# Performance work log

Hardware: AMD Instinct MI355X
Metric: run time of the kernel (lower is better)

## Reference

```python
import jax, jax.numpy as jnp
import numpy as np

N, MAX_NB, H, L, V, B, M = 16384, 15, 512, 128, 1024, 256, 65536


def setup_inputs() -> dict:
    key = jax.random.key(0)
    ks = jax.random.split(key, 32)
    s = 0.02  # param init scale
    inp = {
        'x_ids': jax.random.randint(ks[0], (N,), 0, V, dtype=jnp.int32),
        'contexts': jax.random.randint(ks[1], (N,), 0, B, dtype=jnp.int32),
        'nei_idx': jax.random.randint(ks[2], (N, MAX_NB), 0, M, dtype=jnp.int32),
        'nei_mask': jax.random.randint(ks[3], (N, MAX_NB), 0, 2, dtype=jnp.int32),
        'o_idx': jax.random.randint(ks[4], (N, MAX_NB), 0, M, dtype=jnp.int32),
        'o_mask': jax.random.randint(ks[5], (N, MAX_NB), 0, 2, dtype=jnp.int32),
        'H_msg': jax.random.normal(ks[6], (M, H), jnp.float32),
        'x_tree_vecs': jax.random.normal(ks[7], (B, L), jnp.float32),
        'embedding': jax.random.normal(ks[8], (V, H), jnp.float32) * s,
        'Wz_w': jax.random.normal(ks[9], (H, 2 * H), jnp.float32) * s,
        'Wz_b': jnp.zeros((H,), jnp.float32),
        'Wr_w': jax.random.normal(ks[10], (H, H), jnp.float32) * s,
        'Wr_b': jnp.zeros((H,), jnp.float32),
        'Ur_w': jax.random.normal(ks[11], (H, H), jnp.float32) * s,
        'Wh_w': jax.random.normal(ks[12], (H, 2 * H), jnp.float32) * s,
        'Wh_b': jnp.zeros((H,), jnp.float32),
        'W_w': jax.random.normal(ks[13], (H, H + L), jnp.float32) * s,
        'W_b': jnp.zeros((H,), jnp.float32),
        'Wo_w': jax.random.normal(ks[14], (V, H), jnp.float32) * s,
        'Wo_b': jnp.zeros((V,), jnp.float32),
        'Ui_w': jax.random.normal(ks[15], (H, 2 * H), jnp.float32) * s,
        'Ui_b': jnp.zeros((H,), jnp.float32),
        'U_w': jax.random.normal(ks[16], (H, H + L), jnp.float32) * s,
        'U_b': jnp.zeros((H,), jnp.float32),
        'Uo_w': jax.random.normal(ks[17], (1, H), jnp.float32) * s,
        'Uo_b': jnp.zeros((1,), jnp.float32),
    }
    return inp


def _gru(x, h_nei, Wz_w, Wz_b, Wr_w, Wr_b, Ur_w, Wh_w, Wh_b):
    # x: [N,H], h_nei: [N,MAX_NB,H]
    sum_h = h_nei.sum(axis=1)
    z = jax.nn.sigmoid(jnp.concatenate([x, sum_h], axis=1) @ Wz_w.T + Wz_b)
    r1 = (x @ Wr_w.T + Wr_b)[:, None, :]          # [N,1,H]
    r2 = jnp.einsum('nkh,gh->nkg', h_nei, Ur_w)   # U_r(h_nei), no bias
    r = jax.nn.sigmoid(r1 + r2)
    sum_gated = (r * h_nei).sum(axis=1)
    pre_h = jnp.tanh(jnp.concatenate([x, sum_gated], axis=1) @ Wh_w.T + Wh_b)
    return (1.0 - z) * sum_h + z * pre_h


def reference(x_ids, contexts, nei_idx, nei_mask, o_idx, o_mask, H_msg,
              x_tree_vecs, embedding, Wz_w, Wz_b, Wr_w, Wr_b, Ur_w,
              Wh_w, Wh_b, W_w, W_b, Wo_w, Wo_b, Ui_w, Ui_b, U_w, U_b,
              Uo_w, Uo_b):
    x = embedding[x_ids]                                   # [N,H]
    h_nei = H_msg[nei_idx] * nei_mask[..., None].astype(H_msg.dtype)  # [N,NB,H]
    o_nei = H_msg[o_idx] * o_mask[..., None].astype(H_msg.dtype)
    new_h = _gru(x, h_nei, Wz_w, Wz_b, Wr_w, Wr_b, Ur_w, Wh_w, Wh_b)
    cur_o = o_nei.sum(axis=1)                              # [N,H]
    ctx = x_tree_vecs[contexts]                            # [N,L]
    # word prediction: aggregate(new_h, contexts, x_tree_vecs, 'word')
    w_hid = jax.nn.relu(jnp.concatenate([new_h, ctx], axis=1) @ W_w.T + W_b)
    word_scores = w_hid @ Wo_w.T + Wo_b                    # [N,V]
    # stop prediction: U_i(cat(x, cur_o)) -> aggregate(..., 'stop')
    stop_h = jax.nn.relu(jnp.concatenate([x, cur_o], axis=1) @ Ui_w.T + Ui_b)
    s_hid = jax.nn.relu(jnp.concatenate([stop_h, ctx], axis=1) @ U_w.T + U_b)
    stop_scores = s_hid @ Uo_w.T + Uo_b                    # [N,1]
    return jnp.concatenate([word_scores, stop_scores], axis=1)  # [N,V+1]
```

## Files before the change

kernel.cpp:

```cpp
#include <hip/hip_runtime.h>
#include <hip/hip_bf16.h>

typedef unsigned short u16;
typedef unsigned int u32;
typedef __attribute__((ext_vector_type(8))) short s8v;
typedef __attribute__((ext_vector_type(4))) float f4v;

#define HDIM 512
#define NNODE 16384
#define NB 15

__device__ __forceinline__ u16 f2bu(float x) {
  union { float f; u32 i; } v; v.f = x;
  u32 r = v.i + 0x7FFFu + ((v.i >> 16) & 1u);
  return (u16)(r >> 16);
}
__device__ __forceinline__ float bu2f(u16 u) {
  union { u32 i; float f; } v; v.i = ((u32)u) << 16;
  return v.f;
}
__device__ __forceinline__ u32 pk(float a, float b) {
  return (u32)f2bu(a) | ((u32)f2bu(b) << 16);
}
__device__ __forceinline__ float sigm(float x) {
  return __builtin_amdgcn_rcpf(1.f + __expf(-x));
}
__device__ __forceinline__ void gl16(const void* g, void* l) {
  __builtin_amdgcn_global_load_lds(
      (const __attribute__((address_space(1))) u32*)g,
      (__attribute__((address_space(3))) u32*)l, 16, 0, 0);
}
template<int N> __device__ __forceinline__ void wait_vm() {
  if constexpr (N == 0) asm volatile("s_waitcnt vmcnt(0)" ::: "memory");
  else if constexpr (N == 2) asm volatile("s_waitcnt vmcnt(2)" ::: "memory");
  else asm volatile("s_waitcnt vmcnt(4)" ::: "memory");
}

__global__ __launch_bounds__(256) void k_cvt_all(
    const float* Wz_w, const float* Wr_w, const float* Wh_w, const float* Ui_w,
    const float* Ur_w, const float* W_w, const float* U_w, const float* Wo_w,
    const float* emb, const float* xtree,
    const float* Wz_b, const float* Wr_b, const float* Wh_b, const float* Ui_b,
    const float* W_b, const float* U_b,
    u16* wcat, u16* wz_h, u16* wh_h, u16* ui_h, u16* ur, u16* w_n, u16* u_n,
    u16* ccat, u16* wo, u16* emb_bf, u16* xt_bf, float* ebias, float* cbias) {
  int seg = blockIdx.y;
  const float* src = nullptr; u16* dst = nullptr;
  const float* fsrc = nullptr; float* fdst = nullptr;
  int R = 0, Cs = 0, c0 = 0, C = 0, fn = 0;
  switch (seg) {
    case 0:  src = Wz_w; dst = wcat;              R = 512;  Cs = 1024; c0 = 0;   C = 512; break;
    case 1:  src = Wr_w; dst = wcat + 512 * 512;  R = 512;  Cs = 512;  c0 = 0;   C = 512; break;
    case 2:  src = Wh_w; dst = wcat + 1024 * 512; R = 512;  Cs = 1024; c0 = 0;   C = 512; break;
    case 3:  src = Ui_w; dst = wcat + 1536 * 512; R = 512;  Cs = 1024; c0 = 0;   C = 512; break;
    case 4:  src = Wz_w; dst = wz_h;              R = 512;  Cs = 1024; c0 = 512; C = 512; break;
    case 5:  src = Wh_w; dst = wh_h;              R = 512;  Cs = 1024; c0 = 512; C = 512; break;
    case 6:  src = Ui_w; dst = ui_h;              R = 512;  Cs = 1024; c0 = 512; C = 512; break;
    case 7:  src = Ur_w; dst = ur;                R = 512;  Cs = 512;  c0 = 0;   C = 512; break;
    case 8:  src = W_w;  dst = w_n;               R = 512;  Cs = 640;  c0 = 0;   C = 512; break;
    case 9:  src = U_w;  dst = u_n;               R = 512;  Cs = 640;  c0 = 0;   C = 512; break;
    case 10: src = W_w;  dst = ccat;              R = 512;  Cs = 640;  c0 = 512; C = 128; break;
    case 11: src = U_w;  dst = ccat + 512 * 128;  R = 512;  Cs = 640;  c0 = 512; C = 128; break;
    case 12: src = Wo_w; dst = wo;                R = 1024; Cs = 512;  c0 = 0;   C = 512; break;
    case 13: src = emb;  dst = emb_bf;            R = 1024; Cs = 512;  c0 = 0;   C = 512; break;
    case 14: src = xtree; dst = xt_bf;            R = 256;  Cs = 128;  c0 = 0;   C = 128; break;
    case 15: fsrc = Wz_b; fdst = ebias;        fn = 512; break;
    case 16: fsrc = Wr_b; fdst = ebias + 512;  fn = 512; break;
    case 17: fsrc = Wh_b; fdst = ebias + 1024; fn = 512; break;
    case 18: fsrc = Ui_b; fdst = ebias + 1536; fn = 512; break;
    case 19: fsrc = W_b;  fdst = cbias;        fn = 512; break;
    case 20: fsrc = U_b;  fdst = cbias + 512;  fn = 512; break;
  }
  int i = blockIdx.x * 256 + threadIdx.x;
  if (fdst) { if (i < fn) fdst[i] = fsrc[i]; return; }
  int e0 = i * 8;
  if (e0 >= R * C) return;
  int r = e0 / C, c = e0 - r * C;
  const float* s = src + (size_t)r * Cs + c0 + c;
  float4 a = *reinterpret_cast<const float4*>(s);
  float4 b = *reinterpret_cast<const float4*>(s + 4);
  uint4 o = {pk(a.x, a.y), pk(a.z, a.w), pk(b.x, b.y), pk(b.z, b.w)};
  *reinterpret_cast<uint4*>(&dst[e0]) = o;
}

__global__ void k_cvtH(const float* __restrict__ src, u16* __restrict__ HR) {
  size_t i = ((size_t)blockIdx.x * 256 + threadIdx.x) * 8;
  size_t m = i >> 9, c = i & 511;
  float4 a = *reinterpret_cast<const float4*>(src + i);
  float4 b = *reinterpret_cast<const float4*>(src + i + 4);
  uint4 o = {pk(a.x, a.y), pk(a.z, a.w), pk(b.x, b.y), pk(b.z, b.w)};
  *reinterpret_cast<uint4*>(&HR[m * 1024 + c]) = o;
}

struct GP {
  const u16* A; const u16* B; int K; int lda;
  const float* gadd; int ldg; const int* gidx;
  const float* bias; const u16* shb;
  float* outf; u16* outh; int ldo;
};

template<int EP>
__device__ __forceinline__ void epi(int row, int col, float v, const GP& g) {
  if constexpr (EP == 0) {
    g.outf[(size_t)row * g.ldo + col] = v + (g.bias ? g.bias[col] : 0.f);
  } else if constexpr (EP == 3) {
    float pre = v + g.gadd[(size_t)g.gidx[row] * g.ldg + col];
    g.outh[(size_t)row * g.ldo + col] = f2bu(pre > 0.f ? pre : 0.f);
  } else {
    g.outh[(size_t)row * g.ldo + col] = f2bu(v);
  }
}

template<int EP, int KV>
__device__ void gemm_core(const GP& g, u16* AsB, u16* BsB) {
  const int tid = threadIdx.x, lane = tid & 63, w = tid >> 6;
  const int wm = (w >> 2) * 64, wn = (w & 3) * 32;
  const int nx = gridDim.x;
  int orig = blockIdx.y * nx + blockIdx.x;
  int q = (nx * gridDim.y) >> 3;
  int tile = (orig & 7) * q + (orig >> 3);
  const int n0 = (tile % nx) * 128, m0 = (tile / nx) * 128;

  const int sr = tid >> 2, sc = (tid & 3) ^ (sr & 3);
  const u16* gA = g.A + (size_t)(m0 + sr) * g.lda + sc * 8;
  const u16* gB = g.B + (size_t)(n0 + sr) * KV + sc * 8;
  const int ls = tid * 8;

  f4v acc[4][2];
  f4v z4 = {0.f, 0.f, 0.f, 0.f};
#pragma unroll
  for (int a = 0; a < 4; a++) { acc[a][0] = z4; acc[a][1] = z4; }

  constexpr int T = KV / 32;
  auto STAGE = [&](int t) {
    int buf = (t & 3) * 4096;
    gl16(gA + t * 32, AsB + buf + ls);
    gl16(gB + t * 32, BsB + buf + ls);
  };
  STAGE(0); STAGE(1); STAGE(2);

#pragma unroll
  for (int t = 0; t < T; t++) {
    if (t < T - 2) wait_vm<4>();
    else if (t == T - 2) wait_vm<2>();
    else wait_vm<0>();
    __builtin_amdgcn_s_barrier();
    asm volatile("" ::: "memory");
    if (t + 3 < T) STAGE(t + 3);
    const u16* as = AsB + (t & 3) * 4096;
    const u16* bs = BsB + (t & 3) * 4096;
    s8v af[4], bf[2];
    int cc = lane >> 4;
#pragma unroll
    for (int i = 0; i < 4; i++) {
      int R = wm + i * 16 + (lane & 15);
      af[i] = *reinterpret_cast<const s8v*>(&as[R * 32 + (cc ^ (R & 3)) * 8]);
    }
#pragma unroll
    for (int i = 0; i < 2; i++) {
      int C = wn + i * 16 + (lane & 15);
      bf[i] = *reinterpret_cast<const s8v*>(&bs[C * 32 + (cc ^ (C & 3)) * 8]);
    }
    __builtin_amdgcn_s_setprio(1);
#pragma unroll
    for (int mi = 0; mi < 4; mi++)
#pragma unroll
      for (int ni = 0; ni < 2; ni++)
        acc[mi][ni] = __builtin_amdgcn_mfma_f32_16x16x32_bf16(
            af[mi], bf[ni], acc[mi][ni], 0, 0, 0);
    __builtin_amdgcn_s_setprio(0);
  }
#pragma unroll
  for (int mi = 0; mi < 4; mi++)
#pragma unroll
    for (int ni = 0; ni < 2; ni++)
#pragma unroll
      for (int r = 0; r < 4; r++) {
        int row = m0 + wm + mi * 16 + (lane >> 4) * 4 + r;
        int col = n0 + wn + ni * 16 + (lane & 15);
        epi<EP>(row, col, acc[mi][ni][r], g);
      }
}

template<int EP, int KV>
__global__ __launch_bounds__(512, 4) void k_gemm(GP g) {
  __shared__ u16 As[4 * 4096], Bs[4 * 4096];
  gemm_core<EP, KV>(g, As, Bs);
}

template<int EPa, int EPb, int KV>
__global__ __launch_bounds__(512, 4) void k_pair(GP a, GP b) {
  __shared__ u16 As[4 * 4096], Bs[4 * 4096];
  if (blockIdx.z == 0) gemm_core<EPa, KV>(a, As, Bs);
  else gemm_core<EPb, KV>(b, As, Bs);
}

__global__ __launch_bounds__(512, 4) void k_znp(
    const u16* __restrict__ sumh, const u16* __restrict__ sg,
    const u16* __restrict__ Wz, const u16* __restrict__ Wh,
    const float* __restrict__ E_z, const float* __restrict__ E_h, int ldg,
    const int* __restrict__ gidx, u16* __restrict__ newh, GP gs) {
  __shared__ u16 S[32768];
  if (blockIdx.z == 1) { gemm_core<3, 512>(gs, S, S + 16384); return; }
  u16* As1 = S; u16* Bs1 = S + 8192;
  u16* As2 = S + 16384; u16* Bs2 = S + 24576;
  const int tid = threadIdx.x, lane = tid & 63, w = tid >> 6;
  const int wm = (w >> 2) * 64, wn = (w & 3) * 32;
  const int nx = gridDim.x;
  int orig = blockIdx.y * nx + blockIdx.x;
  int q = (nx * gridDim.y) >> 3;
  int tile = (orig & 7) * q + (orig >> 3);
  const int n0 = (tile % nx) * 128, m0 = (tile / nx) * 128;

  const u16 *gA1[2], *gA2[2], *gB1[2], *gB2[2]; int ls[2];
#pragma unroll
  for (int i = 0; i < 2; i++) {
    int slot = tid + i * 512;
    int r = slot >> 3, c = (slot & 7) ^ (r & 7);
    gA1[i] = sumh + (size_t)(m0 + r) * HDIM + c * 8;
    gA2[i] = sg + (size_t)(m0 + r) * HDIM + c * 8;
    gB1[i] = Wz + (size_t)(n0 + r) * HDIM + c * 8;
    gB2[i] = Wh + (size_t)(n0 + r) * HDIM + c * 8;
    ls[i] = slot * 8;
  }

  f4v az[4][2], ah[4][2];
  f4v z4 = {0.f, 0.f, 0.f, 0.f};
#pragma unroll
  for (int a = 0; a < 4; a++) {
    az[a][0] = z4; az[a][1] = z4; ah[a][0] = z4; ah[a][1] = z4;
  }

  for (int k0 = 0; k0 < HDIM; k0 += 64) {
    __syncthreads();
#pragma unroll
    for (int i = 0; i < 2; i++) gl16(gA1[i] + k0, As1 + ls[i]);
#pragma unroll
    for (int i = 0; i < 2; i++) gl16(gB1[i] + k0, Bs1 + ls[i]);
#pragma unroll
    for (int i = 0; i < 2; i++) gl16(gA2[i] + k0, As2 + ls[i]);
#pragma unroll
    for (int i = 0; i < 2; i++) gl16(gB2[i] + k0, Bs2 + ls[i]);
    __syncthreads();
#pragma unroll
    for (int ks = 0; ks < 2; ks++) {
      int cc = ks * 4 + (lane >> 4);
      {
        s8v af[4], bf[2];
#pragma unroll
        for (int i = 0; i < 4; i++) {
          int R = wm + i * 16 + (lane & 15);
          af[i] = *reinterpret_cast<const s8v*>(&As1[R * 64 + (cc ^ (R & 7)) * 8]);
        }
#pragma unroll
        for (int i = 0; i < 2; i++) {
          int C = wn + i * 16 + (lane & 15);
          bf[i] = *reinterpret_cast<const s8v*>(&Bs1[C * 64 + (cc ^ (C & 7)) * 8]);
        }
        __builtin_amdgcn_s_setprio(1);
#pragma unroll
        for (int mi = 0; mi < 4; mi++)
#pragma unroll
          for (int ni = 0; ni < 2; ni++)
            az[mi][ni] = __builtin_amdgcn_mfma_f32_16x16x32_bf16(
                af[mi], bf[ni], az[mi][ni], 0, 0, 0);
        __builtin_amdgcn_s_setprio(0);
      }
      {
        s8v af[4], bf[2];
#pragma unroll
        for (int i = 0; i < 4; i++) {
          int R = wm + i * 16 + (lane & 15);
          af[i] = *reinterpret_cast<const s8v*>(&As2[R * 64 + (cc ^ (R & 7)) * 8]);
        }
#pragma unroll
        for (int i = 0; i < 2; i++) {
          int C = wn + i * 16 + (lane & 15);
          bf[i] = *reinterpret_cast<const s8v*>(&Bs2[C * 64 + (cc ^ (C & 7)) * 8]);
        }
        __builtin_amdgcn_s_setprio(1);
#pragma unroll
        for (int mi = 0; mi < 4; mi++)
#pragma unroll
          for (int ni = 0; ni < 2; ni++)
            ah[mi][ni] = __builtin_amdgcn_mfma_f32_16x16x32_bf16(
                af[mi], bf[ni], ah[mi][ni], 0, 0, 0);
        __builtin_amdgcn_s_setprio(0);
      }
    }
  }
#pragma unroll
  for (int mi = 0; mi < 4; mi++)
#pragma unroll
    for (int r = 0; r < 4; r++) {
      int row = m0 + wm + mi * 16 + (lane >> 4) * 4 + r;
      int xid = gidx[row];
      const float* ez = E_z + (size_t)xid * ldg;
      const float* eh = E_h + (size_t)xid * ldg;
#pragma unroll
      for (int ni = 0; ni < 2; ni++) {
        int col = n0 + wn + ni * 16 + (lane & 15);
        float zv = sigm(az[mi][ni][r] + ez[col]);
        float pre = tanhf(ah[mi][ni][r] + eh[col]);
        float sh = bu2f(sumh[(size_t)row * HDIM + col]);
        newh[(size_t)row * HDIM + col] = f2bu((1.f - zv) * sh + zv * pre);
      }
    }
}

__global__ __launch_bounds__(256) void k_gsr(
    const u16* __restrict__ HR,
    const float* __restrict__ E_r, int ldg, const int* __restrict__ x_ids,
    const int* __restrict__ nei_idx, const int* __restrict__ nei_mask,
    const int* __restrict__ o_idx, const int* __restrict__ o_mask,
    u16* __restrict__ sum_h_bf, u16* __restrict__ sg_bf,
    u16* __restrict__ cur_o_bf) {
  int t = threadIdx.x;
  int nd = t >> 6, lane = t & 63;
  int n = blockIdx.x * 4 + nd;
  __shared__ int sidx[4][NB], smsk[4][NB], soid[4][NB], somk[4][NB];
  __shared__ int sx[4];
  if (t < 60) {
    int nn = t / 15, k = t - nn * 15;
    size_t gofs = (size_t)(blockIdx.x * 4 + nn) * NB + k;
    sidx[nn][k] = nei_idx[gofs];
    smsk[nn][k] = nei_mask[gofs];
  } else if (t >= 64 && t < 124) {
    int tt = t - 64;
    int nn = tt / 15, k = tt - nn * 15;
    size_t gofs = (size_t)(blockIdx.x * 4 + nn) * NB + k;
    soid[nn][k] = o_idx[gofs];
    somk[nn][k] = o_mask[gofs];
  } else if (t >= 128 && t < 132) {
    sx[t - 128] = x_ids[blockIdx.x * 4 + (t - 128)];
  }
  __syncthreads();
  int c = lane * 8;
  const float* er = E_r + (size_t)sx[nd] * ldg + c;
  float4 e0 = *reinterpret_cast<const float4*>(er);
  float4 e1 = *reinterpret_cast<const float4*>(er + 4);
  float ev[8] = {e0.x, e0.y, e0.z, e0.w, e1.x, e1.y, e1.z, e1.w};
  float s[8], gg[8], oo[8];
#pragma unroll
  for (int i = 0; i < 8; i++) { s[i] = 0.f; gg[i] = 0.f; oo[i] = 0.f; }
#pragma unroll
  for (int k = 0; k < NB; k++) {
    if (smsk[nd][k]) {
      const u16* row = HR + (size_t)sidx[nd][k] * 1024 + c;
      uint4 hv = *reinterpret_cast<const uint4*>(row);
      uint4 rv = *reinterpret_cast<const uint4*>(row + 512);
      u32 ha[4] = {hv.x, hv.y, hv.z, hv.w};
      u32 ra[4] = {rv.x, rv.y, rv.z, rv.w};
#pragma unroll
      for (int p = 0; p < 4; p++) {
        float h0 = bu2f((u16)ha[p]), h1 = bu2f((u16)(ha[p] >> 16));
        s[p * 2] += h0; s[p * 2 + 1] += h1;
        gg[p * 2] += sigm(bu2f((u16)ra[p]) + ev[p * 2]) * h0;
        gg[p * 2 + 1] += sigm(bu2f((u16)(ra[p] >> 16)) + ev[p * 2 + 1]) * h1;
      }
    }
    if (somk[nd][k]) {
      uint4 ov = *reinterpret_cast<const uint4*>(
          HR + (size_t)soid[nd][k] * 1024 + c);
      u32 oa[4] = {ov.x, ov.y, ov.z, ov.w};
#pragma unroll
      for (int p = 0; p < 4; p++) {
        oo[p * 2] += bu2f((u16)oa[p]);
        oo[p * 2 + 1] += bu2f((u16)(oa[p] >> 16));
      }
    }
  }
  size_t b = (size_t)n * HDIM + c;
  uint4 ps = {pk(s[0], s[1]), pk(s[2], s[3]), pk(s[4], s[5]), pk(s[6], s[7])};
  uint4 pg = {pk(gg[0], gg[1]), pk(gg[2], gg[3]), pk(gg[4], gg[5]), pk(gg[6], gg[7])};
  uint4 po = {pk(oo[0], oo[1]), pk(oo[2], oo[3]), pk(oo[4], oo[5]), pk(oo[6], oo[7])};
  *reinterpret_cast<uint4*>(&sum_h_bf[b]) = ps;
  *reinterpret_cast<uint4*>(&sg_bf[b]) = pg;
  *reinterpret_cast<uint4*>(&cur_o_bf[b]) = po;
}

__global__ __launch_bounds__(512, 4) void k_wordstop(
    GP wgp, const u16* __restrict__ shid, const float* __restrict__ Uo_w,
    const float* __restrict__ Uo_b, float* __restrict__ out) {
  __shared__ u16 As[4 * 4096], Bs[4 * 4096];
  if (blockIdx.z == 0) { gemm_core<0, 512>(wgp, As, Bs); return; }
  int b = blockIdx.y * gridDim.x + blockIdx.x;
  int wv = threadIdx.x >> 6, lane = threadIdx.x & 63;
#pragma unroll
  for (int i = 0; i < 2; i++) {
    int n = b * 16 + wv * 2 + i;
    const u16* row = shid + (size_t)n * HDIM + lane * 8;
    const float* uw = Uo_w + lane * 8;
    uint4 v = *reinterpret_cast<const uint4*>(row);
    float4 u0 = *reinterpret_cast<const float4*>(uw);
    float4 u1 = *reinterpret_cast<const float4*>(uw + 4);
    float s = bu2f((u16)v.x) * u0.x + bu2f((u16)(v.x >> 16)) * u0.y +
              bu2f((u16)v.y) * u0.z + bu2f((u16)(v.y >> 16)) * u0.w +
              bu2f((u16)v.z) * u1.x + bu2f((u16)(v.z >> 16)) * u1.y +
              bu2f((u16)v.w) * u1.z + bu2f((u16)(v.w >> 16)) * u1.w;
#pragma unroll
    for (int off = 32; off; off >>= 1) s += __shfl_xor(s, off, 64);
    if (lane == 0) out[(size_t)n * 1025 + 1024] = s + Uo_b[0];
  }
}

extern "C" void kernel_launch(void* const* d_in, const int* in_sizes, int n_in,
                              void* d_out, int out_size, void* d_ws, size_t ws_size,
                              hipStream_t stream) {
  const int* x_ids = (const int*)d_in[0];
  const int* contexts = (const int*)d_in[1];
  const int* nei_idx = (const int*)d_in[2];
  const int* nei_mask = (const int*)d_in[3];
  const int* o_idx = (const int*)d_in[4];
  const int* o_mask = (const int*)d_in[5];
  const float* H_msg = (const float*)d_in[6];
  const float* xtree = (const float*)d_in[7];
  const float* emb = (const float*)d_in[8];
  const float* Wz_w = (const float*)d_in[9];  const float* Wz_b = (const float*)d_in[10];
  const float* Wr_w = (const float*)d_in[11]; const float* Wr_b = (const float*)d_in[12];
  const float* Ur_w = (const float*)d_in[13];
  const float* Wh_w = (const float*)d_in[14]; const float* Wh_b = (const float*)d_in[15];
  const float* W_w  = (const float*)d_in[16]; const float* W_b  = (const float*)d_in[17];
  const float* Wo_w = (const float*)d_in[18]; const float* Wo_b = (const float*)d_in[19];
  const float* Ui_w = (const float*)d_in[20]; const float* Ui_b = (const float*)d_in[21];
  const float* U_w  = (const float*)d_in[22]; const float* U_b  = (const float*)d_in[23];
  const float* Uo_w = (const float*)d_in[24]; const float* Uo_b = (const float*)d_in[25];
  float* out = (float*)d_out;
  const int M = 65536;

  char* base = (char*)d_ws;
  size_t ofs = 0;
  auto alloc = [&](size_t bytes) -> char* {
    char* p = base + ofs;
    ofs = (ofs + bytes + 255) & ~(size_t)255;
    return p;
  };
  u16* wcat  = (u16*)alloc((size_t)2048 * 512 * 2);
  u16* wz_h  = (u16*)alloc(512 * 512 * 2);
  u16* wh_h  = (u16*)alloc(512 * 512 * 2);
  u16* ui_h  = (u16*)alloc(512 * 512 * 2);
  u16* ur    = (u16*)alloc(512 * 512 * 2);
  u16* w_n   = (u16*)alloc(512 * 512 * 2);
  u16* u_n   = (u16*)alloc(512 * 512 * 2);
  u16* ccat  = (u16*)alloc(1024 * 128 * 2);
  u16* wo    = (u16*)alloc(1024 * 512 * 2);
  u16* emb_bf = (u16*)alloc(1024 * 512 * 2);
  u16* xt_bf  = (u16*)alloc(256 * 128 * 2);
  float* ebias = (float*)alloc(2048 * 4);
  float* cbias = (float*)alloc(1024 * 4);
  float* E_cat = (float*)alloc((size_t)1024 * 2048 * 4);
  float* C_cat = (float*)alloc((size_t)256 * 1024 * 4);
  u16* HR = (u16*)alloc((size_t)M * 1024 * 2);
  u16* sum_h_bf = (u16*)alloc((size_t)NNODE * HDIM * 2);
  u16* cur_o_bf = (u16*)alloc((size_t)NNODE * HDIM * 2);
  u16* sg_bf    = (u16*)alloc((size_t)NNODE * HDIM * 2);
  u16* newh_bf  = (u16*)alloc((size_t)NNODE * HDIM * 2);
  u16* whid_bf  = (u16*)alloc((size_t)NNODE * HDIM * 2);
  u16* stoph_bf = (u16*)alloc((size_t)NNODE * HDIM * 2);
  u16* shid_bf  = (u16*)alloc((size_t)NNODE * HDIM * 2);

  k_cvt_all<<<dim3(256, 21), dim3(256), 0, stream>>>(
      Wz_w, Wr_w, Wh_w, Ui_w, Ur_w, W_w, U_w, Wo_w, emb, xtree,
      Wz_b, Wr_b, Wh_b, Ui_b, W_b, U_b,
      wcat, wz_h, wh_h, ui_h, ur, w_n, u_n, ccat, wo, emb_bf, xt_bf,
      ebias, cbias);
  k_cvtH<<<dim3(16384), dim3(256), 0, stream>>>(H_msg, HR);

  GP ge{emb_bf, wcat, 512, 512, nullptr, 0, nullptr, ebias, nullptr,
        E_cat, nullptr, 2048};
  k_gemm<0, 512><<<dim3(16, 8), dim3(512), 0, stream>>>(ge);
  GP gc{xt_bf, ccat, 128, 128, nullptr, 0, nullptr, cbias, nullptr,
        C_cat, nullptr, 1024};
  k_gemm<0, 128><<<dim3(8, 2), dim3(512), 0, stream>>>(gc);

  GP gr{HR, ur, 512, 1024, nullptr, 0, nullptr, nullptr, nullptr,
        nullptr, HR + 512, 1024};
  k_gemm<4, 512><<<dim3(4, 512), dim3(512), 0, stream>>>(gr);

  k_gsr<<<dim3(NNODE / 4), dim3(256), 0, stream>>>(
      HR, E_cat + 512, 2048, x_ids, nei_idx, nei_mask, o_idx, o_mask,
      sum_h_bf, sg_bf, cur_o_bf);

  GP gs{cur_o_bf, ui_h, 512, 512, E_cat + 1536, 2048, x_ids, nullptr, nullptr,
        nullptr, stoph_bf, 512};
  k_znp<<<dim3(4, 128, 2), dim3(512), 0, stream>>>(
      sum_h_bf, sg_bf, wz_h, wh_h, E_cat, E_cat + 1024, 2048, x_ids,
      newh_bf, gs);

  GP gw{newh_bf, w_n, 512, 512, C_cat, 1024, contexts, nullptr, nullptr,
        nullptr, whid_bf, 512};
  GP gu{stoph_bf, u_n, 512, 512, C_cat + 512, 1024, contexts, nullptr, nullptr,
        nullptr, shid_bf, 512};
  k_pair<3, 3, 512><<<dim3(4, 128, 2), dim3(512), 0, stream>>>(gw, gu);

  GP gword{whid_bf, wo, 512, 512, nullptr, 0, nullptr, Wo_b, nullptr,
           out, nullptr, 1025};
  k_wordstop<<<dim3(8, 128, 2), dim3(512), 0, stream>>>(
      gword, shid_bf, Uo_w, Uo_b, out);
}
```

Before: 320.1 us.

## Split fused GRU z/h dual-GEMM into three-way GEMM launch plus elementwise kernel

Replaces the custom dual-accumulator k_znp kernel, which computed the z and h pre-activations together and applied the GRU update in its epilogue. The z and h GEMMs now run as separate blocks in a three-way launch alongside the stop GEMM, writing bf16 intermediates, and a new vectorized elementwise kernel applies sigmoid, tanh and the gate blend. The aim is to use the generic pipelined gemm_core, with lower register and LDS pressure per block, and to balance work across z-slices. In exchange it adds 32 MB of extra global traffic plus one extra launch, and rounds the pre-activations to bf16 before the nonlinearity.

```diff
diff --git a/kernel.cpp b/kernel.cpp
--- a/kernel.cpp
+++ b/kernel.cpp
@@ -195,117 +195,47 @@
   else gemm_core<EPb, KV>(b, As, Bs);
 }
 
-__global__ __launch_bounds__(512, 4) void k_znp(
-    const u16* __restrict__ sumh, const u16* __restrict__ sg,
-    const u16* __restrict__ Wz, const u16* __restrict__ Wh,
-    const float* __restrict__ E_z, const float* __restrict__ E_h, int ldg,
-    const int* __restrict__ gidx, u16* __restrict__ newh, GP gs) {
-  __shared__ u16 S[32768];
-  if (blockIdx.z == 1) { gemm_core<3, 512>(gs, S, S + 16384); return; }
-  u16* As1 = S; u16* Bs1 = S + 8192;
-  u16* As2 = S + 16384; u16* Bs2 = S + 24576;
-  const int tid = threadIdx.x, lane = tid & 63, w = tid >> 6;
-  const int wm = (w >> 2) * 64, wn = (w & 3) * 32;
-  const int nx = gridDim.x;
-  int orig = blockIdx.y * nx + blockIdx.x;
-  int q = (nx * gridDim.y) >> 3;
-  int tile = (orig & 7) * q + (orig >> 3);
-  const int n0 = (tile % nx) * 128, m0 = (tile / nx) * 128;
-
-  const u16 *gA1[2], *gA2[2], *gB1[2], *gB2[2]; int ls[2];
-#pragma unroll
-  for (int i = 0; i < 2; i++) {
-    int slot = tid + i * 512;
-    int r = slot >> 3, c = (slot & 7) ^ (r & 7);
-    gA1[i] = sumh + (size_t)(m0 + r) * HDIM + c * 8;
-    gA2[i] = sg + (size_t)(m0 + r) * HDIM + c * 8;
-    gB1[i] = Wz + (size_t)(n0 + r) * HDIM + c * 8;
-    gB2[i] = Wh + (size_t)(n0 + r) * HDIM + c * 8;
-    ls[i] = slot * 8;
-  }
-
-  f4v az[4][2], ah[4][2];
-  f4v z4 = {0.f, 0.f, 0.f, 0.f};
-#pragma unroll
-  for (int a = 0; a < 4; a++) {
-    az[a][0] = z4; az[a][1] = z4; ah[a][0] = z4; ah[a][1] = z4;
-  }
-
-  for (int k0 = 0; k0 < HDIM; k0 += 64) {
-    __syncthreads();
-#pragma unroll
-    for (int i = 0; i < 2; i++) gl16(gA1[i] + k0, As1 + ls[i]);
-#pragma unroll
-    for (int i = 0; i < 2; i++) gl16(gB1[i] + k0, Bs1 + ls[i]);
-#pragma unroll
-    for (int i = 0; i < 2; i++) gl16(gA2[i] + k0, As2 + ls[i]);
-#pragma unroll
-    for (int i = 0; i < 2; i++) gl16(gB2[i] + k0, Bs2 + ls[i]);
-    __syncthreads();
-#pragma unroll
-    for (int ks = 0; ks < 2; ks++) {
-      int cc = ks * 4 + (lane >> 4);
-      {
-        s8v af[4], bf[2];
-#pragma unroll
-        for (int i = 0; i < 4; i++) {
-          int R = wm + i * 16 + (lane & 15);
-          af[i] = *reinterpret_cast<const s8v*>(&As1[R * 64 + (cc ^ (R & 7)) * 8]);
-        }
-#pragma unroll
-        for (int i = 0; i < 2; i++) {
-          int C = wn + i * 16 + (lane & 15);
-          bf[i] = *reinterpret_cast<const s8v*>(&Bs1[C * 64 + (cc ^ (C & 7)) * 8]);
-        }
-        __builtin_amdgcn_s_setprio(1);
-#pragma unroll
-        for (int mi = 0; mi < 4; mi++)
-#pragma unroll
-          for (int ni = 0; ni < 2; ni++)
-            az[mi][ni] = __builtin_amdgcn_mfma_f32_16x16x32_bf16(
-                af[mi], bf[ni], az[mi][ni], 0, 0, 0);
-        __builtin_amdgcn_s_setprio(0);
-      }
-      {
-        s8v af[4], bf[2];
-#pragma unroll
-        for (int i = 0; i < 4; i++) {
-          int R = wm + i * 16 + (lane & 15);
-          af[i] = *reinterpret_cast<const s8v*>(&As2[R * 64 + (cc ^ (R & 7)) * 8]);
-        }
-#pragma unroll
-        for (int i = 0; i < 2; i++) {
-          int C = wn + i * 16 + (lane & 15);
-          bf[i] = *reinterpret_cast<const s8v*>(&Bs2[C * 64 + (cc ^ (C & 7)) * 8]);
-        }
-        __builtin_amdgcn_s_setprio(1);
-#pragma unroll
-        for (int mi = 0; mi < 4; mi++)
-#pragma unroll
-          for (int ni = 0; ni < 2; ni++)
-            ah[mi][ni] = __builtin_amdgcn_mfma_f32_16x16x32_bf16(
-                af[mi], bf[ni], ah[mi][ni], 0, 0, 0);
-        __builtin_amdgcn_s_setprio(0);
-      }
-    }
-  }
-#pragma unroll
-  for (int mi = 0; mi < 4; mi++)
-#pragma unroll
-    for (int r = 0; r < 4; r++) {
-      int row = m0 + wm + mi * 16 + (lane >> 4) * 4 + r;
-      int xid = gidx[row];
-      const float* ez = E_z + (size_t)xid * ldg;
-      const float* eh = E_h + (size_t)xid * ldg;
-#pragma unroll
-      for (int ni = 0; ni < 2; ni++) {
-        int col = n0 + wn + ni * 16 + (lane & 15);
-        float zv = sigm(az[mi][ni][r] + ez[col]);
-        float pre = tanhf(ah[mi][ni][r] + eh[col]);
-        float sh = bu2f(sumh[(size_t)row * HDIM + col]);
-        newh[(size_t)row * HDIM + col] = f2bu((1.f - zv) * sh + zv * pre);
-      }
-    }
+template<int EPa, int EPb, int EPc, int KV>
+__global__ __launch_bounds__(512, 4) void k_trip(GP a, GP b, GP c) {
+  __shared__ u16 As[4 * 4096], Bs[4 * 4096];
+  if (blockIdx.z == 0) gemm_core<EPa, KV>(a, As, Bs);
+  else if (blockIdx.z == 1) gemm_core<EPb, KV>(b, As, Bs);
+  else gemm_core<EPc, KV>(c, As, Bs);
+}
+
+__global__ __launch_bounds__(256) void k_newh(
+    const u16* __restrict__ az, const u16* __restrict__ ah,
+    const u16* __restrict__ sumh, const float* __restrict__ E_cat,
+    const int* __restrict__ x_ids, u16* __restrict__ newh) {
+  size_t i = ((size_t)blockIdx.x * 256 + threadIdx.x) * 8;
+  int row = (int)(i >> 9), c = (int)(i & 511);
+  int xid = x_ids[row];
+  const float* ez = E_cat + (size_t)xid * 2048 + c;
+  const float* eh = ez + 1024;
+  uint4 a4 = *reinterpret_cast<const uint4*>(az + i);
+  uint4 h4 = *reinterpret_cast<const uint4*>(ah + i);
+  uint4 s4 = *reinterpret_cast<const uint4*>(sumh + i);
+  float4 ez0 = *reinterpret_cast<const float4*>(ez);
+  float4 ez1 = *reinterpret_cast<const float4*>(ez + 4);
+  float4 eh0 = *reinterpret_cast<const float4*>(eh);
+  float4 eh1 = *reinterpret_cast<const float4*>(eh + 4);
+  float eza[8] = {ez0.x, ez0.y, ez0.z, ez0.w, ez1.x, ez1.y, ez1.z, ez1.w};
+  float eha[8] = {eh0.x, eh0.y, eh0.z, eh0.w, eh1.x, eh1.y, eh1.z, eh1.w};
+  u32 aa[4] = {a4.x, a4.y, a4.z, a4.w};
+  u32 hh[4] = {h4.x, h4.y, h4.z, h4.w};
+  u32 ss[4] = {s4.x, s4.y, s4.z, s4.w};
+  u32 outw[4];
+#pragma unroll
+  for (int p = 0; p < 4; p++) {
+    float z0 = sigm(bu2f((u16)aa[p]) + eza[p * 2]);
+    float z1 = sigm(bu2f((u16)(aa[p] >> 16)) + eza[p * 2 + 1]);
+    float p0 = tanhf(bu2f((u16)hh[p]) + eha[p * 2]);
+    float p1 = tanhf(bu2f((u16)(hh[p] >> 16)) + eha[p * 2 + 1]);
+    float sh0 = bu2f((u16)ss[p]), sh1 = bu2f((u16)(ss[p] >> 16));
+    outw[p] = pk((1.f - z0) * sh0 + z0 * p0, (1.f - z1) * sh1 + z1 * p1);
+  }
+  uint4 o = {outw[0], outw[1], outw[2], outw[3]};
+  *reinterpret_cast<uint4*>(newh + i) = o;
 }
 
 __global__ __launch_bounds__(256) void k_gsr(
@@ -454,6 +384,8 @@
   u16* sum_h_bf = (u16*)alloc((size_t)NNODE * HDIM * 2);
   u16* cur_o_bf = (u16*)alloc((size_t)NNODE * HDIM * 2);
   u16* sg_bf    = (u16*)alloc((size_t)NNODE * HDIM * 2);
+  u16* az_bf    = (u16*)alloc((size_t)NNODE * HDIM * 2);
+  u16* ah_bf    = (u16*)alloc((size_t)NNODE * HDIM * 2);
   u16* newh_bf  = (u16*)alloc((size_t)NNODE * HDIM * 2);
   u16* whid_bf  = (u16*)alloc((size_t)NNODE * HDIM * 2);
   u16* stoph_bf = (u16*)alloc((size_t)NNODE * HDIM * 2);
@@ -481,11 +413,16 @@
       HR, E_cat + 512, 2048, x_ids, nei_idx, nei_mask, o_idx, o_mask,
       sum_h_bf, sg_bf, cur_o_bf);
 
+  GP gaz{sum_h_bf, wz_h, 512, 512, nullptr, 0, nullptr, nullptr, nullptr,
+         nullptr, az_bf, 512};
+  GP gah{sg_bf, wh_h, 512, 512, nullptr, 0, nullptr, nullptr, nullptr,
+         nullptr, ah_bf, 512};
   GP gs{cur_o_bf, ui_h, 512, 512, E_cat + 1536, 2048, x_ids, nullptr, nullptr,
         nullptr, stoph_bf, 512};
-  k_znp<<<dim3(4, 128, 2), dim3(512), 0, stream>>>(
-      sum_h_bf, sg_bf, wz_h, wh_h, E_cat, E_cat + 1024, 2048, x_ids,
-      newh_bf, gs);
+  k_trip<4, 4, 3, 512><<<dim3(4, 128, 3), dim3(512), 0, stream>>>(gaz, gah, gs);
+
+  k_newh<<<dim3(4096), dim3(256), 0, stream>>>(
+      az_bf, ah_bf, sum_h_bf, E_cat, x_ids, newh_bf);
 
   GP gw{newh_bf, w_n, 512, 512, C_cat, 1024, contexts, nullptr, nullptr,
         nullptr, whid_bf, 512};
```

After: 338.3 us. 5.7% more time.

## Double-buffer the z/h dual GEMM in k_znp with K=32 stages

Applied to the files above, without the earlier changes.

Restructures the k_znp dual-GEMM main loop from single-buffered K=64 tiles, with two barriers per step, to double-buffered K=32 tiles with one barrier per step. The next stage's global-to-LDS loads are issued before computing the current stage, so memory latency can overlap MFMA work. The same LDS budget is reused and the swizzle is adapted to the 32-wide rows. The trade-off is twice as many iterations and smaller per-stage work. It also relies on a single barrier to protect buffer reuse.

```diff
diff --git a/kernel.cpp b/kernel.cpp
--- a/kernel.cpp
+++ b/kernel.cpp
@@ -202,8 +202,6 @@
     const int* __restrict__ gidx, u16* __restrict__ newh, GP gs) {
   __shared__ u16 S[32768];
   if (blockIdx.z == 1) { gemm_core<3, 512>(gs, S, S + 16384); return; }
-  u16* As1 = S; u16* Bs1 = S + 8192;
-  u16* As2 = S + 16384; u16* Bs2 = S + 24576;
   const int tid = threadIdx.x, lane = tid & 63, w = tid >> 6;
   const int wm = (w >> 2) * 64, wn = (w & 3) * 32;
   const int nx = gridDim.x;
@@ -212,17 +210,20 @@
   int tile = (orig & 7) * q + (orig >> 3);
   const int n0 = (tile % nx) * 128, m0 = (tile / nx) * 128;
 
-  const u16 *gA1[2], *gA2[2], *gB1[2], *gB2[2]; int ls[2];
-#pragma unroll
-  for (int i = 0; i < 2; i++) {
-    int slot = tid + i * 512;
-    int r = slot >> 3, c = (slot & 7) ^ (r & 7);
-    gA1[i] = sumh + (size_t)(m0 + r) * HDIM + c * 8;
-    gA2[i] = sg + (size_t)(m0 + r) * HDIM + c * 8;
-    gB1[i] = Wz + (size_t)(n0 + r) * HDIM + c * 8;
-    gB2[i] = Wh + (size_t)(n0 + r) * HDIM + c * 8;
-    ls[i] = slot * 8;
-  }
+  const int sr = tid >> 2, sc = (tid & 3) ^ (sr & 3);
+  const u16* gA1 = sumh + (size_t)(m0 + sr) * HDIM + sc * 8;
+  const u16* gA2 = sg + (size_t)(m0 + sr) * HDIM + sc * 8;
+  const u16* gB1 = Wz + (size_t)(n0 + sr) * HDIM + sc * 8;
+  const u16* gB2 = Wh + (size_t)(n0 + sr) * HDIM + sc * 8;
+  const int ls = tid * 8;
+  auto STAGE = [&](int t) {
+    u16* base = S + (t & 1) * 16384;
+    int k0 = t * 32;
+    gl16(gA1 + k0, base + ls);
+    gl16(gB1 + k0, base + 4096 + ls);
+    gl16(gA2 + k0, base + 8192 + ls);
+    gl16(gB2 + k0, base + 12288 + ls);
+  };
 
   f4v az[4][2], ah[4][2];
   f4v z4 = {0.f, 0.f, 0.f, 0.f};
@@ -231,62 +232,56 @@
     az[a][0] = z4; az[a][1] = z4; ah[a][0] = z4; ah[a][1] = z4;
   }
 
-  for (int k0 = 0; k0 < HDIM; k0 += 64) {
+  STAGE(0);
+#pragma unroll
+  for (int t = 0; t < 16; t++) {
     __syncthreads();
-#pragma unroll
-    for (int i = 0; i < 2; i++) gl16(gA1[i] + k0, As1 + ls[i]);
-#pragma unroll
-    for (int i = 0; i < 2; i++) gl16(gB1[i] + k0, Bs1 + ls[i]);
-#pragma unroll
-    for (int i = 0; i < 2; i++) gl16(gA2[i] + k0, As2 + ls[i]);
-#pragma unroll
-    for (int i = 0; i < 2; i++) gl16(gB2[i] + k0, Bs2 + ls[i]);
-    __syncthreads();
-#pragma unroll
-    for (int ks = 0; ks < 2; ks++) {
-      int cc = ks * 4 + (lane >> 4);
-      {
-        s8v af[4], bf[2];
-#pragma unroll
-        for (int i = 0; i < 4; i++) {
-          int R = wm + i * 16 + (lane & 15);
-          af[i] = *reinterpret_cast<const s8v*>(&As1[R * 64 + (cc ^ (R & 7)) * 8]);
-        }
-#pragma unroll
-        for (int i = 0; i < 2; i++) {
-          int C = wn + i * 16 + (lane & 15);
-          bf[i] = *reinterpret_cast<const s8v*>(&Bs1[C * 64 + (cc ^ (C & 7)) * 8]);
-        }
-        __builtin_amdgcn_s_setprio(1);
-#pragma unroll
-        for (int mi = 0; mi < 4; mi++)
-#pragma unroll
-          for (int ni = 0; ni < 2; ni++)
-            az[mi][ni] = __builtin_amdgcn_mfma_f32_16x16x32_bf16(
-                af[mi], bf[ni], az[mi][ni], 0, 0, 0);
-        __builtin_amdgcn_s_setprio(0);
-      }
-      {
-        s8v af[4], bf[2];
-#pragma unroll
-        for (int i = 0; i < 4; i++) {
-          int R = wm + i * 16 + (lane & 15);
-          af[i] = *reinterpret_cast<const s8v*>(&As2[R * 64 + (cc ^ (R & 7)) * 8]);
-        }
-#pragma unroll
-        for (int i = 0; i < 2; i++) {
-          int C = wn + i * 16 + (lane & 15);
-          bf[i] = *reinterpret_cast<const s8v*>(&Bs2[C * 64 + (cc ^ (C & 7)) * 8]);
-        }
-        __builtin_amdgcn_s_setprio(1);
-#pragma unroll
-        for (int mi = 0; mi < 4; mi++)
-#pragma unroll
-          for (int ni = 0; ni < 2; ni++)
-            ah[mi][ni] = __builtin_amdgcn_mfma_f32_16x16x32_bf16(
-                af[mi], bf[ni], ah[mi][ni], 0, 0, 0);
-        __builtin_amdgcn_s_setprio(0);
-      }
+    if (t + 1 < 16) STAGE(t + 1);
+    const u16* base = S + (t & 1) * 16384;
+    const u16* As1 = base, *Bs1 = base + 4096;
+    const u16* As2 = base + 8192, *Bs2 = base + 12288;
+    int cc = lane >> 4;
+    {
+      s8v af[4], bf[2];
+#pragma unroll
+      for (int i = 0; i < 4; i++) {
+        int R = wm + i * 16 + (lane & 15);
+        af[i] = *reinterpret_cast<const s8v*>(&As1[R * 32 + (cc ^ (R & 3)) * 8]);
+      }
+#pragma unroll
+      for (int i = 0; i < 2; i++) {
+        int C = wn + i * 16 + (lane & 15);
+        bf[i] = *reinterpret_cast<const s8v*>(&Bs1[C * 32 + (cc ^ (C & 3)) * 8]);
+      }
+      __builtin_amdgcn_s_setprio(1);
+#pragma unroll
+      for (int mi = 0; mi < 4; mi++)
+#pragma unroll
+        for (int ni = 0; ni < 2; ni++)
+          az[mi][ni] = __builtin_amdgcn_mfma_f32_16x16x32_bf16(
+              af[mi], bf[ni], az[mi][ni], 0, 0, 0);
+      __builtin_amdgcn_s_setprio(0);
+    }
+    {
+      s8v af[4], bf[2];
+#pragma unroll
+      for (int i = 0; i < 4; i++) {
+        int R = wm + i * 16 + (lane & 15);
+        af[i] = *reinterpret_cast<const s8v*>(&As2[R * 32 + (cc ^ (R & 3)) * 8]);
+      }
+#pragma unroll
+      for (int i = 0; i < 2; i++) {
+        int C = wn + i * 16 + (lane & 15);
+        bf[i] = *reinterpret_cast<const s8v*>(&Bs2[C * 32 + (cc ^ (C & 3)) * 8]);
+      }
+      __builtin_amdgcn_s_setprio(1);
+#pragma unroll
+      for (int mi = 0; mi < 4; mi++)
+#pragma unroll
+        for (int ni = 0; ni < 2; ni++)
+          ah[mi][ni] = __builtin_amdgcn_mfma_f32_16x16x32_bf16(
+              af[mi], bf[ni], ah[mi][ni], 0, 0, 0);
+      __builtin_amdgcn_s_setprio(0);
     }
   }
 #pragma unroll
```

Result: no change. 319.1 us (-0.3%).
